# Performance work log

Measured on AMD Instinct MI355X. Metric: run time of the kernel, lower is better.

Reference implementation:

```python
import jax, jax.numpy as jnp
import numpy as np

B, G = 64, 48            # events, grid side -> N = B*G*G nodes
N = B * G * G
DIMS = [128, 102, 73, 44, 16]   # channel schedule from GraphZ defaults
KERN = 3                 # GMM kernels on the conv layer
MAXV = 1.0               # Cartesian(max_value=neighbors=1)


def _build_graph():
    # 3x3 window graph (radius 1, self loops) per event, as in window_edges
    ix, iy = np.meshgrid(np.arange(G), np.arange(G), indexing='ij')
    ix, iy = ix.ravel(), iy.ravel()
    srcs, tgts = [], []
    for dx in (-1, 0, 1):
        for dy in (-1, 0, 1):
            jx, jy = ix + dx, iy + dy
            m = (jx >= 0) & (jx < G) & (jy >= 0) & (jy < G)
            srcs.append(jx[m] * G + jy[m])
            tgts.append(ix[m] * G + iy[m])
    src, tgt = np.concatenate(srcs), np.concatenate(tgts)
    base = (np.arange(B) * G * G)[:, None]
    ei = np.stack([(base + src[None]).ravel(), (base + tgt[None]).ravel()])
    pos = np.stack([np.tile(ix, B).astype(np.float32),
                    np.tile(iy, B).astype(np.float32),
                    np.repeat(np.arange(B), G * G).astype(np.float32)], axis=1)
    return ei.astype(np.int32), pos


def setup_inputs() -> dict:
    key = jax.random.key(0)
    ks = jax.random.split(key, 16)
    ei, pos = _build_graph()
    inp = {
        'x': jax.random.normal(ks[0], (N, DIMS[0]), jnp.float32),
        'pos': jnp.asarray(pos),
        'edge_index': jnp.asarray(ei),
    }
    # pointwise layer 0: 128->102 (+BN)
    inp['w0'] = jax.random.normal(ks[1], (DIMS[0], DIMS[1]), jnp.float32) * (1.0 / np.sqrt(DIMS[0]))
    inp['b0'] = jnp.zeros((DIMS[1],), jnp.float32)
    inp['gamma0'] = jnp.ones((DIMS[1],), jnp.float32)
    inp['beta0'] = jnp.zeros((DIMS[1],), jnp.float32)
    # pointwise layer 1: 102->73 (+BN)
    inp['w1'] = jax.random.normal(ks[2], (DIMS[1], DIMS[2]), jnp.float32) * (1.0 / np.sqrt(DIMS[1]))
    inp['b1'] = jnp.zeros((DIMS[2],), jnp.float32)
    inp['gamma1'] = jnp.ones((DIMS[2],), jnp.float32)
    inp['beta1'] = jnp.zeros((DIMS[2],), jnp.float32)
    # GMM conv layer 2: 73->44, 3 gaussian kernels (+BN)
    inp['w2'] = jax.random.normal(ks[3], (DIMS[2], DIMS[3]), jnp.float32) * (1.0 / np.sqrt(DIMS[2]))
    inp['g2'] = jax.random.normal(ks[4], (DIMS[2], KERN * DIMS[3]), jnp.float32) * (1.0 / np.sqrt(DIMS[2]))
    inp['mu2'] = jax.random.uniform(ks[5], (KERN, 2), jnp.float32)
    inp['sigma2'] = jax.random.uniform(ks[6], (KERN, 2), jnp.float32) + 0.5
    inp['b2'] = jnp.zeros((DIMS[3],), jnp.float32)
    inp['gamma2'] = jnp.ones((DIMS[3],), jnp.float32)
    inp['beta2'] = jnp.zeros((DIMS[3],), jnp.float32)
    # pointwise layer 3: 44->16
    inp['w3'] = jax.random.normal(ks[7], (DIMS[3], DIMS[4]), jnp.float32) * (1.0 / np.sqrt(DIMS[3]))
    inp['b3'] = jnp.zeros((DIMS[4],), jnp.float32)
    return inp


def _bn(x, gamma, beta):
    # BatchNorm1d training forward: biased batch stats over the node dim
    m = jnp.mean(x, axis=0)
    v = jnp.mean((x - m) ** 2, axis=0)
    return (x - m) * jax.lax.rsqrt(v + 1e-5) * gamma + beta


def _gmm_conv(x, ei, ea, g, mu, sigma, w_root, b, n):
    # PyG GMMConv (separate_gaussians=False, aggr='mean', root_weight, bias)
    E = ea.shape[0]
    kk = mu.shape[0]
    out = w_root.shape[1]
    xj = (x @ g)[ei[0]].reshape(E, kk, out)                 # gather transformed src feats
    gauss = jnp.exp(jnp.sum(-0.5 * (ea[:, None, :] - mu[None]) ** 2
                            / (1e-15 + sigma[None] ** 2), axis=-1))  # [E, K]
    msg = jnp.einsum('eko,ek->eo', xj, gauss)               # [E, out]
    s = jax.ops.segment_sum(msg, ei[1], num_segments=n)     # scatter-add to targets
    c = jax.ops.segment_sum(jnp.ones((E,), x.dtype), ei[1], num_segments=n)
    return s / jnp.maximum(c, 1.0)[:, None] + x @ w_root + b


def reference(x, pos, edge_index, w0, b0, gamma0, beta0, w1, b1, gamma1, beta1,
              w2, g2, mu2, sigma2, b2, gamma2, beta2, w3, b3):
    n = x.shape[0]
    pos2 = pos[:, :2]
    # Cartesian(max_value=1, norm=True): pseudo coords in [0, 1]
    ea = (pos2[edge_index[0]] - pos2[edge_index[1]]) / (2.0 * MAXV) + 0.5
    # layers 0,1: knn_graph(k=0) -> empty edge set -> GMMConv = root Linear + bias
    h = _bn(x @ w0 + b0, gamma0, beta0)
    h = _bn(h @ w1 + b1, gamma1, beta1)
    # layer 2: window-edge GMMConv with 3 gaussian kernels
    h = _bn(_gmm_conv(h, edge_index, ea, g2, mu2, sigma2, w2, b2, n), gamma2, beta2)
    # layer 3: pointwise, no norm
    return h @ w3 + b3
```

## Files before the change

kernel.cpp:

```cpp
#include <hip/hip_runtime.h>

#define GRIDW 48
#define NNODES 147456
#define NTILES 2304
#define GB 512

typedef __attribute__((ext_vector_type(8))) short short8;
typedef __attribute__((ext_vector_type(4))) float f32x4;

__device__ inline unsigned short f2bf(float f) {
    union { float f; unsigned u; } v; v.f = f;
    unsigned r = v.u + 0x7FFFu + ((v.u >> 16) & 1u);
    return (unsigned short)(r >> 16);
}
__device__ inline float bf2f(unsigned short h) {
    union { unsigned u; float f; } v; v.u = ((unsigned)h) << 16;
    return v.f;
}

__global__ void prep(const float* __restrict__ w0, const float* __restrict__ b0,
                     const float* __restrict__ w1, const float* __restrict__ b1,
                     const float* __restrict__ g2, const float* __restrict__ w2,
                     const float* __restrict__ b2, const float* __restrict__ w3,
                     const float* __restrict__ b3,
                     unsigned short* __restrict__ wt0, unsigned short* __restrict__ wt1,
                     unsigned short* __restrict__ wt2, unsigned short* __restrict__ wt3,
                     float* __restrict__ biasf0, float* __restrict__ biasf1,
                     float* __restrict__ biasf2, float* __restrict__ biasf3,
                     float* __restrict__ statz) {
    int id = blockIdx.x * 256 + threadIdx.x;
    if (id < 14336) {
        int col = id >> 7, k = id & 127;
        wt0[id] = (col < 102) ? f2bf(w0[k * 102 + col]) : (unsigned short)0;
    } else if (id < 24576) {
        int e = id - 14336; int col = e >> 7, k = e & 127;
        wt1[e] = (col < 73 && k < 102) ? f2bf(w1[k * 73 + col]) : (unsigned short)0;
    } else if (id < 41472) {
        int e = id - 24576; int col = e / 96, k = e - (e / 96) * 96;
        unsigned short v = 0;
        if (k < 73) v = (col < 132) ? f2bf(g2[k * 132 + col]) : f2bf(w2[k * 44 + (col - 132)]);
        wt2[e] = v;
    } else if (id < 42496) {
        int e = id - 41472; int col = e >> 6, k = e & 63;
        wt3[e] = (k < 44) ? f2bf(w3[k * 16 + col]) : (unsigned short)0;
    } else if (id < 42608) { int c = id - 42496; biasf0[c] = (c < 102) ? b0[c] : 0.f; }
    else if (id < 42688) { int c = id - 42608; biasf1[c] = (c < 73) ? b1[c] : 0.f; }
    else if (id < 42864) { int c = id - 42688; biasf2[c] = (c < 132) ? 0.f : b2[c - 132]; }
    else if (id < 42880) { int c = id - 42864; biasf3[c] = b3[c]; }
    else if (id < 43392) { statz[id - 42880] = 0.f; }
}

template<int K, int KP, int MP, int MOUT, int PREVM, int BNSRC,
         bool STATS, bool OUTBF, bool ABF16>
__global__ __launch_bounds__(256) void gemm_p(
    const void* __restrict__ Ain, const unsigned short* __restrict__ WT,
    const float* __restrict__ biasf,
    const float* __restrict__ q0, const float* __restrict__ q1,
    const float* __restrict__ q2, const float* __restrict__ q3,
    float invN, void* __restrict__ Yout,
    float* __restrict__ sumO, float* __restrict__ ssO)
{
    constexpr int KS = KP + 8;
    constexpr int NCF = MP / 16;
    constexpr int UPR = ABF16 ? (K / 8) : (K / 4);
    constexpr int TOT = 64 * UPR;
    constexpr int NLD = (TOT + 255) / 256;
    __shared__ __align__(16) unsigned short As[2][64 * KS];
    __shared__ __align__(16) unsigned short Bs[MP * KS];
    __shared__ float bnA[KP], bnB[KP];

    const int tid = threadIdx.x;
    const int lane = tid & 63, wv = tid >> 6, qd = lane >> 4, lc = lane & 15;

    if (BNSRC == 1) {
        if (tid < KP) {
            float a = 0.f, b = 0.f;
            if (tid < PREVM) {
                float m = q0[tid] * invN;
                float v = q1[tid] * invN - m * m;
                float sc = q2[tid] * rsqrtf(v + 1e-5f);
                a = sc; b = q3[tid] - m * sc;
            }
            bnA[tid] = a; bnB[tid] = b;
        }
    } else if (BNSRC == 2) {
        if (tid < KP) {
            bnA[tid] = (tid < PREVM) ? q0[tid] : 0.f;
            bnB[tid] = (tid < PREVM) ? q1[tid] : 0.f;
        }
    }
    for (int g = tid; g < MP * (KP / 8); g += 256) {
        int col = g / (KP / 8), u = g - col * (KP / 8);
        *(uint4*)&Bs[col * KS + u * 8] = *(const uint4*)&WT[(size_t)col * KP + u * 8];
    }
    if constexpr (KP > K) {
        constexpr int PADU = (KP - K) / 2;
        for (int g = tid; g < 64 * PADU; g += 256) {
            int row = g / PADU, u = g - row * PADU;
            *(unsigned*)&As[0][row * KS + K + u * 2] = 0u;
            *(unsigned*)&As[1][row * KS + K + u * 2] = 0u;
        }
    }

    float bvr[NCF];
#pragma unroll
    for (int cf = 0; cf < NCF; ++cf) bvr[cf] = biasf[cf * 16 + lc];

    float cs[NCF], cq[NCF];
    if (STATS) {
#pragma unroll
        for (int cf = 0; cf < NCF; ++cf) { cs[cf] = 0.f; cq[cf] = 0.f; }
    }

    uint4 pfb[NLD];
    float4 pff[NLD];

    int t = blockIdx.x;
#pragma unroll
    for (int i = 0; i < NLD; ++i) {
        int g = tid + 256 * i;
        if (g < TOT) {
            if constexpr (ABF16)
                pfb[i] = *(const uint4*)((const unsigned short*)Ain + (size_t)t * 64 * K + g * 8);
            else
                pff[i] = *(const float4*)((const float*)Ain + (size_t)t * 64 * K + g * 4);
        }
    }
    __syncthreads();

    int buf = 0;
    for (; t < NTILES; t += GB) {
#pragma unroll
        for (int i = 0; i < NLD; ++i) {
            int g = tid + 256 * i;
            if (g < TOT) {
                int row = g / UPR, u = g - row * UPR;
                if constexpr (ABF16) {
                    uint4 w = pfb[i];
                    if (BNSRC != 0) {
                        unsigned* wp = (unsigned*)&w;
#pragma unroll
                        for (int pp = 0; pp < 4; ++pp) {
                            int kk = u * 8 + 2 * pp;
                            float lo = bf2f((unsigned short)(wp[pp] & 0xFFFFu)) * bnA[kk] + bnB[kk];
                            float hi = bf2f((unsigned short)(wp[pp] >> 16)) * bnA[kk + 1] + bnB[kk + 1];
                            wp[pp] = (unsigned)f2bf(lo) | ((unsigned)f2bf(hi) << 16);
                        }
                    }
                    *(uint4*)&As[buf][row * KS + u * 8] = w;
                } else {
                    float4 v = pff[i];
                    if (BNSRC != 0) {
                        int kk = u * 4;
                        v.x = v.x * bnA[kk] + bnB[kk];
                        v.y = v.y * bnA[kk + 1] + bnB[kk + 1];
                        v.z = v.z * bnA[kk + 2] + bnB[kk + 2];
                        v.w = v.w * bnA[kk + 3] + bnB[kk + 3];
                    }
                    unsigned lo = (unsigned)f2bf(v.x) | ((unsigned)f2bf(v.y) << 16);
                    unsigned hi = (unsigned)f2bf(v.z) | ((unsigned)f2bf(v.w) << 16);
                    *(uint2*)&As[buf][row * KS + u * 4] = make_uint2(lo, hi);
                }
            }
        }
        int t2 = t + GB;
        if (t2 < NTILES) {
#pragma unroll
            for (int i = 0; i < NLD; ++i) {
                int g = tid + 256 * i;
                if (g < TOT) {
                    if constexpr (ABF16)
                        pfb[i] = *(const uint4*)((const unsigned short*)Ain + (size_t)t2 * 64 * K + g * 8);
                    else
                        pff[i] = *(const float4*)((const float*)Ain + (size_t)t2 * 64 * K + g * 4);
                }
            }
        }
        __syncthreads();

        f32x4 acc[NCF];
#pragma unroll
        for (int cf = 0; cf < NCF; ++cf) acc[cf] = (f32x4){0.f, 0.f, 0.f, 0.f};
#pragma unroll
        for (int kt = 0; kt < KP / 32; ++kt) {
            const int kb = kt * 32 + qd * 8;
            short8 a = *(const short8*)&As[buf][(wv * 16 + lc) * KS + kb];
#pragma unroll
            for (int cf = 0; cf < NCF; ++cf) {
                short8 b = *(const short8*)&Bs[(cf * 16 + lc) * KS + kb];
                acc[cf] = __builtin_amdgcn_mfma_f32_16x16x32_bf16(a, b, acc[cf], 0, 0, 0);
            }
        }
#pragma unroll
        for (int cf = 0; cf < NCF; ++cf) {
            const int col = cf * 16 + lc;
            const float bv = bvr[cf];
#pragma unroll
            for (int rr = 0; rr < 4; ++rr) {
                float v = acc[cf][rr] + bv;
                int row = t * 64 + wv * 16 + qd * 4 + rr;
                if (OUTBF) ((unsigned short*)Yout)[(size_t)row * MP + col] = f2bf(v);
                else       ((float*)Yout)[(size_t)row * MP + col] = v;
                if (STATS) { cs[cf] += v; cq[cf] += v * v; }
            }
        }
        buf ^= 1;
    }

    if (STATS) {
        __syncthreads();
        float* red = (float*)As;
        float* redq = red + 4 * MP;
#pragma unroll
        for (int cf = 0; cf < NCF; ++cf) {
            float s = cs[cf], qq = cq[cf];
            s += __shfl_down(s, 32, 64); s += __shfl_down(s, 16, 64);
            qq += __shfl_down(qq, 32, 64); qq += __shfl_down(qq, 16, 64);
            if (lane < 16) {
                red[wv * MP + cf * 16 + lane] = s;
                redq[wv * MP + cf * 16 + lane] = qq;
            }
        }
        __syncthreads();
        if (tid < MOUT) {
            float s = red[tid] + red[MP + tid] + red[2 * MP + tid] + red[3 * MP + tid];
            float qq = redq[tid] + redq[MP + tid] + redq[2 * MP + tid] + redq[3 * MP + tid];
            atomicAdd(&sumO[tid], s);
            atomicAdd(&ssO[tid], qq);
        }
    }
}

__device__ inline void load_u(const unsigned short* __restrict__ TR, int b,
                              int jx, int iy, int c0, const float (*gy)[3],
                              float* __restrict__ u) {
#pragma unroll
    for (int j = 0; j < 12; ++j) u[j] = 0.f;
    if (jx < 0 || jx >= GRIDW) return;
    const unsigned short* rowp = TR + (size_t)(b * 2304 + jx * 48) * 176;
#pragma unroll
    for (int dy = -1; dy <= 1; ++dy) {
        int jy = iy + dy;
        if (jy < 0 || jy >= GRIDW) continue;
        const unsigned short* np = rowp + (size_t)jy * 176 + c0;
#pragma unroll
        for (int k = 0; k < 3; ++k) {
            uint2 v = *(const uint2*)(np + k * 44);
            float g = gy[dy + 1][k];
            u[k * 4 + 0] += g * bf2f((unsigned short)(v.x & 0xFFFFu));
            u[k * 4 + 1] += g * bf2f((unsigned short)(v.x >> 16));
            u[k * 4 + 2] += g * bf2f((unsigned short)(v.y & 0xFFFFu));
            u[k * 4 + 3] += g * bf2f((unsigned short)(v.y >> 16));
        }
    }
}

__global__ __launch_bounds__(256) void gmm_stencil(
    const unsigned short* __restrict__ TR, unsigned short* __restrict__ C,
    const float* __restrict__ mu, const float* __restrict__ sigma,
    float* __restrict__ sum2, float* __restrict__ ss2)
{
    __shared__ float gx[3][3], gy[3][3];
    __shared__ float red[88];
    const int tid = threadIdx.x;
    if (tid < 88) red[tid] = 0.f;
    if (tid < 18) {
        int d = (tid / 3) % 3, k = tid % 3;
        bool isy = tid >= 9;
        float e = 0.5f * (float)(d - 1) + 0.5f;
        float mm = mu[k * 2 + (isy ? 1 : 0)];
        float sg = sigma[k * 2 + (isy ? 1 : 0)];
        float v = expf(-0.5f * (e - mm) * (e - mm) / (1e-15f + sg * sg));
        if (isy) gy[d][k] = v; else gx[d][k] = v;
    }
    __syncthreads();

    const int r = blockIdx.x & 7;
    const int m = blockIdx.x >> 3;
    const int b = r * 8 + (m >> 4);
    const int x0 = (m & 15) * 3;

    for (int p = 0; p < 3; ++p) {
        int idx = tid + 256 * p;
        if (idx >= 528) break;
        int og = idx % 11, iy = idx / 11;
        int c0 = og * 4;
        float u0[12], u1[12], u2[12];
        load_u(TR, b, x0 - 1, iy, c0, gy, u0);
        load_u(TR, b, x0,     iy, c0, gy, u1);
        float s4[4] = {0, 0, 0, 0}, q4[4] = {0, 0, 0, 0};
        int ny = 1 + (iy > 0) + (iy < GRIDW - 1);
#pragma unroll
        for (int st = 0; st < 3; ++st) {
            int ix = x0 + st;
            float* ua = (st == 0) ? u0 : ((st == 1) ? u1 : u2);
            float* ub = (st == 0) ? u1 : ((st == 1) ? u2 : u0);
            float* uc = (st == 0) ? u2 : ((st == 1) ? u0 : u1);
            load_u(TR, b, ix + 1, iy, c0, gy, uc);
            int nx = 1 + (ix > 0) + (ix < GRIDW - 1);
            float inv = 1.f / (float)(nx * ny);
            int node = b * 2304 + ix * 48 + iy;
            uint2 rv = *(const uint2*)(TR + (size_t)node * 176 + 132 + c0);
            float o[4];
#pragma unroll
            for (int j = 0; j < 4; ++j) {
                float acc = 0.f;
#pragma unroll
                for (int k = 0; k < 3; ++k)
                    acc += gx[0][k] * ua[k * 4 + j] + gx[1][k] * ub[k * 4 + j]
                         + gx[2][k] * uc[k * 4 + j];
                o[j] = acc * inv;
            }
            o[0] += bf2f((unsigned short)(rv.x & 0xFFFFu));
            o[1] += bf2f((unsigned short)(rv.x >> 16));
            o[2] += bf2f((unsigned short)(rv.y & 0xFFFFu));
            o[3] += bf2f((unsigned short)(rv.y >> 16));
            unsigned lo = (unsigned)f2bf(o[0]) | ((unsigned)f2bf(o[1]) << 16);
            unsigned hi = (unsigned)f2bf(o[2]) | ((unsigned)f2bf(o[3]) << 16);
            *(uint2*)&C[(size_t)node * 48 + c0] = make_uint2(lo, hi);
            if (og == 10)
                *(uint2*)&C[(size_t)node * 48 + 44] = make_uint2(0u, 0u);
#pragma unroll
            for (int j = 0; j < 4; ++j) { s4[j] += o[j]; q4[j] += o[j] * o[j]; }
        }
#pragma unroll
        for (int j = 0; j < 4; ++j) {
            atomicAdd(&red[c0 + j], s4[j]);
            atomicAdd(&red[44 + c0 + j], q4[j]);
        }
    }
    __syncthreads();
    if (tid < 88)
        atomicAdd(tid < 44 ? &sum2[tid] : &ss2[tid - 44], red[tid]);
}

extern "C" void kernel_launch(void* const* d_in, const int* in_sizes, int n_in,
                              void* d_out, int out_size, void* d_ws, size_t ws_size,
                              hipStream_t stream) {
    const float* x      = (const float*)d_in[0];
    const float* w0     = (const float*)d_in[3];
    const float* b0     = (const float*)d_in[4];
    const float* gamma0 = (const float*)d_in[5];
    const float* beta0  = (const float*)d_in[6];
    const float* w1     = (const float*)d_in[7];
    const float* b1     = (const float*)d_in[8];
    const float* gamma1 = (const float*)d_in[9];
    const float* beta1  = (const float*)d_in[10];
    const float* w2     = (const float*)d_in[11];
    const float* g2     = (const float*)d_in[12];
    const float* mu2    = (const float*)d_in[13];
    const float* sigma2 = (const float*)d_in[14];
    const float* b2     = (const float*)d_in[15];
    const float* gamma2 = (const float*)d_in[16];
    const float* beta2  = (const float*)d_in[17];
    const float* w3     = (const float*)d_in[18];
    const float* b3     = (const float*)d_in[19];
    float* out = (float*)d_out;

    const int N = NNODES;
    const float invN = 1.0f / (float)N;

    const size_t tailOff = (size_t)N * 132;
    size_t need = (tailOff + 300000) * sizeof(float);
    if (ws_size < need) return;

    float* ws = (float*)d_ws;
    unsigned short* bufY1 = (unsigned short*)ws;
    unsigned short* bufC  = (unsigned short*)ws;
    unsigned short* bufY0 = (unsigned short*)(ws + (size_t)N * 44);
    unsigned short* bufTR = bufY0;

    float* tail = ws + tailOff;
    float* sum0 = tail;
    float* ss0  = tail + 112;
    float* sum1 = tail + 224;
    float* ss1  = tail + 304;
    float* sum2 = tail + 384;
    float* ss2  = tail + 448;
    float* biasf0 = tail + 512;
    float* biasf1 = tail + 624;
    float* biasf2 = tail + 704;
    float* biasf3 = tail + 880;
    unsigned short* wt0 = (unsigned short*)(tail + 896);
    unsigned short* wt1 = wt0 + 14336;
    unsigned short* wt2 = wt1 + 10240;
    unsigned short* wt3 = wt2 + 16896;

    prep<<<170, 256, 0, stream>>>(w0, b0, w1, b1, g2, w2, b2, w3, b3,
                                  wt0, wt1, wt2, wt3,
                                  biasf0, biasf1, biasf2, biasf3, tail);

    gemm_p<128, 128, 112, 102, 0, 0, true, true, false><<<GB, 256, 0, stream>>>(
        x, wt0, biasf0, nullptr, nullptr, nullptr, nullptr, invN, bufY0, sum0, ss0);

    gemm_p<112, 128, 80, 73, 102, 1, true, true, true><<<GB, 256, 0, stream>>>(
        bufY0, wt1, biasf1, sum0, ss0, gamma0, beta0, invN, bufY1, sum1, ss1);

    gemm_p<80, 96, 176, 176, 73, 1, false, true, true><<<GB, 256, 0, stream>>>(
        bufY1, wt2, biasf2, sum1, ss1, gamma1, beta1, invN, bufTR, nullptr, nullptr);

    gmm_stencil<<<1024, 256, 0, stream>>>(bufTR, bufC, mu2, sigma2, sum2, ss2);

    gemm_p<48, 64, 16, 16, 44, 1, false, false, true><<<GB, 256, 0, stream>>>(
        bufC, wt3, biasf3, sum2, ss2, gamma2, beta2, invN, out, nullptr, nullptr);
}
```

Before: 276.0 us.

## Shard BN statistic atomics across 8 slots and flatten stencil grid

BatchNorm sum and sum-of-squares accumulators are split into 8 shards indexed by block id, and consumers add the shards back together when computing mean and variance. This spreads global atomic contention across more addresses. The GMM stencil kernel now maps one work item per thread and launches 2112 blocks instead of 1024 blocks each looping three times, which raises parallelism and removes the idle tail iteration. The cost is a larger zeroed stats area and a few extra loads per BN consumer.

```diff
diff --git a/kernel.cpp b/kernel.cpp
--- a/kernel.cpp
+++ b/kernel.cpp
@@ -4,6 +4,8 @@
 #define NNODES 147456
 #define NTILES 2304
 #define GB 512
+#define NSH 8
+#define SHS 128
 
 typedef __attribute__((ext_vector_type(8))) short short8;
 typedef __attribute__((ext_vector_type(4))) float f32x4;
@@ -47,7 +49,7 @@
     else if (id < 42688) { int c = id - 42608; biasf1[c] = (c < 73) ? b1[c] : 0.f; }
     else if (id < 42864) { int c = id - 42688; biasf2[c] = (c < 132) ? 0.f : b2[c - 132]; }
     else if (id < 42880) { int c = id - 42864; biasf3[c] = b3[c]; }
-    else if (id < 43392) { statz[id - 42880] = 0.f; }
+    else if (id < 49024) { statz[id - 42880] = 0.f; }
 }
 
 template<int K, int KP, int MP, int MOUT, int PREVM, int BNSRC,
@@ -76,17 +78,18 @@
         if (tid < KP) {
             float a = 0.f, b = 0.f;
             if (tid < PREVM) {
-                float m = q0[tid] * invN;
-                float v = q1[tid] * invN - m * m;
+                float s0 = 0.f, s1 = 0.f;
+#pragma unroll
+                for (int sh = 0; sh < NSH; ++sh) {
+                    s0 += q0[sh * SHS + tid];
+                    s1 += q1[sh * SHS + tid];
+                }
+                float m = s0 * invN;
+                float v = s1 * invN - m * m;
                 float sc = q2[tid] * rsqrtf(v + 1e-5f);
                 a = sc; b = q3[tid] - m * sc;
             }
             bnA[tid] = a; bnB[tid] = b;
-        }
-    } else if (BNSRC == 2) {
-        if (tid < KP) {
-            bnA[tid] = (tid < PREVM) ? q0[tid] : 0.f;
-            bnB[tid] = (tid < PREVM) ? q1[tid] : 0.f;
         }
     }
     for (int g = tid; g < MP * (KP / 8); g += 256) {
@@ -225,8 +228,9 @@
         if (tid < MOUT) {
             float s = red[tid] + red[MP + tid] + red[2 * MP + tid] + red[3 * MP + tid];
             float qq = redq[tid] + redq[MP + tid] + redq[2 * MP + tid] + redq[3 * MP + tid];
-            atomicAdd(&sumO[tid], s);
-            atomicAdd(&ssO[tid], qq);
+            const int sh = blockIdx.x & (NSH - 1);
+            atomicAdd(&sumO[sh * SHS + tid], s);
+            atomicAdd(&ssO[sh * SHS + tid], qq);
         }
     }
 }
@@ -275,63 +279,65 @@
     }
     __syncthreads();
 
-    const int r = blockIdx.x & 7;
-    const int m = blockIdx.x >> 3;
-    const int b = r * 8 + (m >> 4);
-    const int x0 = (m & 15) * 3;
-
-    for (int p = 0; p < 3; ++p) {
-        int idx = tid + 256 * p;
-        if (idx >= 528) break;
-        int og = idx % 11, iy = idx / 11;
-        int c0 = og * 4;
-        float u0[12], u1[12], u2[12];
-        load_u(TR, b, x0 - 1, iy, c0, gy, u0);
-        load_u(TR, b, x0,     iy, c0, gy, u1);
-        float s4[4] = {0, 0, 0, 0}, q4[4] = {0, 0, 0, 0};
-        int ny = 1 + (iy > 0) + (iy < GRIDW - 1);
-#pragma unroll
-        for (int st = 0; st < 3; ++st) {
-            int ix = x0 + st;
-            float* ua = (st == 0) ? u0 : ((st == 1) ? u1 : u2);
-            float* ub = (st == 0) ? u1 : ((st == 1) ? u2 : u0);
-            float* uc = (st == 0) ? u2 : ((st == 1) ? u0 : u1);
-            load_u(TR, b, ix + 1, iy, c0, gy, uc);
-            int nx = 1 + (ix > 0) + (ix < GRIDW - 1);
-            float inv = 1.f / (float)(nx * ny);
-            int node = b * 2304 + ix * 48 + iy;
-            uint2 rv = *(const uint2*)(TR + (size_t)node * 176 + 132 + c0);
-            float o[4];
-#pragma unroll
-            for (int j = 0; j < 4; ++j) {
-                float acc = 0.f;
-#pragma unroll
-                for (int k = 0; k < 3; ++k)
-                    acc += gx[0][k] * ua[k * 4 + j] + gx[1][k] * ub[k * 4 + j]
-                         + gx[2][k] * uc[k * 4 + j];
-                o[j] = acc * inv;
-            }
-            o[0] += bf2f((unsigned short)(rv.x & 0xFFFFu));
-            o[1] += bf2f((unsigned short)(rv.x >> 16));
-            o[2] += bf2f((unsigned short)(rv.y & 0xFFFFu));
-            o[3] += bf2f((unsigned short)(rv.y >> 16));
-            unsigned lo = (unsigned)f2bf(o[0]) | ((unsigned)f2bf(o[1]) << 16);
-            unsigned hi = (unsigned)f2bf(o[2]) | ((unsigned)f2bf(o[3]) << 16);
-            *(uint2*)&C[(size_t)node * 48 + c0] = make_uint2(lo, hi);
-            if (og == 10)
-                *(uint2*)&C[(size_t)node * 48 + 44] = make_uint2(0u, 0u);
-#pragma unroll
-            for (int j = 0; j < 4; ++j) { s4[j] += o[j]; q4[j] += o[j] * o[j]; }
-        }
+    const int xcd = blockIdx.x & 7;
+    const int bi  = blockIdx.x >> 3;
+    const int b   = xcd * 8 + bi / 33;
+    const unsigned tau = (unsigned)(bi % 33) * 256u + (unsigned)tid;
+    const int og = (int)(tau % 11u);
+    const unsigned r1 = tau / 11u;
+    const int iy = (int)(r1 % 48u);
+    const int x0 = (int)(r1 / 48u) * 3;
+    const int c0 = og * 4;
+
+    float u0[12], u1[12], u2[12];
+    load_u(TR, b, x0 - 1, iy, c0, gy, u0);
+    load_u(TR, b, x0,     iy, c0, gy, u1);
+    float s4[4] = {0, 0, 0, 0}, q4[4] = {0, 0, 0, 0};
+    int ny = 1 + (iy > 0) + (iy < GRIDW - 1);
+#pragma unroll
+    for (int st = 0; st < 3; ++st) {
+        int ix = x0 + st;
+        float* ua = (st == 0) ? u0 : ((st == 1) ? u1 : u2);
+        float* ub = (st == 0) ? u1 : ((st == 1) ? u2 : u0);
+        float* uc = (st == 0) ? u2 : ((st == 1) ? u0 : u1);
+        load_u(TR, b, ix + 1, iy, c0, gy, uc);
+        int nx = 1 + (ix > 0) + (ix < GRIDW - 1);
+        float inv = 1.f / (float)(nx * ny);
+        int node = b * 2304 + ix * 48 + iy;
+        uint2 rv = *(const uint2*)(TR + (size_t)node * 176 + 132 + c0);
+        float o[4];
 #pragma unroll
         for (int j = 0; j < 4; ++j) {
-            atomicAdd(&red[c0 + j], s4[j]);
-            atomicAdd(&red[44 + c0 + j], q4[j]);
-        }
+            float acc = 0.f;
+#pragma unroll
+            for (int k = 0; k < 3; ++k)
+                acc += gx[0][k] * ua[k * 4 + j] + gx[1][k] * ub[k * 4 + j]
+                     + gx[2][k] * uc[k * 4 + j];
+            o[j] = acc * inv;
+        }
+        o[0] += bf2f((unsigned short)(rv.x & 0xFFFFu));
+        o[1] += bf2f((unsigned short)(rv.x >> 16));
+        o[2] += bf2f((unsigned short)(rv.y & 0xFFFFu));
+        o[3] += bf2f((unsigned short)(rv.y >> 16));
+        unsigned lo = (unsigned)f2bf(o[0]) | ((unsigned)f2bf(o[1]) << 16);
+        unsigned hi = (unsigned)f2bf(o[2]) | ((unsigned)f2bf(o[3]) << 16);
+        *(uint2*)&C[(size_t)node * 48 + c0] = make_uint2(lo, hi);
+        if (og == 10)
+            *(uint2*)&C[(size_t)node * 48 + 44] = make_uint2(0u, 0u);
+#pragma unroll
+        for (int j = 0; j < 4; ++j) { s4[j] += o[j]; q4[j] += o[j] * o[j]; }
+    }
+#pragma unroll
+    for (int j = 0; j < 4; ++j) {
+        atomicAdd(&red[c0 + j], s4[j]);
+        atomicAdd(&red[44 + c0 + j], q4[j]);
     }
     __syncthreads();
-    if (tid < 88)
-        atomicAdd(tid < 44 ? &sum2[tid] : &ss2[tid - 44], red[tid]);
+    if (tid < 88) {
+        const int sh = blockIdx.x & (NSH - 1);
+        if (tid < 44) atomicAdd(&sum2[sh * SHS + tid], red[tid]);
+        else          atomicAdd(&ss2[sh * SHS + tid - 44], red[tid]);
+    }
 }
 
 extern "C" void kernel_launch(void* const* d_in, const int* in_sizes, int n_in,
@@ -372,21 +378,21 @@
 
     float* tail = ws + tailOff;
     float* sum0 = tail;
-    float* ss0  = tail + 112;
-    float* sum1 = tail + 224;
-    float* ss1  = tail + 304;
-    float* sum2 = tail + 384;
-    float* ss2  = tail + 448;
-    float* biasf0 = tail + 512;
-    float* biasf1 = tail + 624;
-    float* biasf2 = tail + 704;
-    float* biasf3 = tail + 880;
-    unsigned short* wt0 = (unsigned short*)(tail + 896);
+    float* ss0  = tail + 1024;
+    float* sum1 = tail + 2048;
+    float* ss1  = tail + 3072;
+    float* sum2 = tail + 4096;
+    float* ss2  = tail + 5120;
+    float* biasf0 = tail + 6144;
+    float* biasf1 = tail + 6256;
+    float* biasf2 = tail + 6336;
+    float* biasf3 = tail + 6512;
+    unsigned short* wt0 = (unsigned short*)(tail + 6528);
     unsigned short* wt1 = wt0 + 14336;
     unsigned short* wt2 = wt1 + 10240;
     unsigned short* wt3 = wt2 + 16896;
 
-    prep<<<170, 256, 0, stream>>>(w0, b0, w1, b1, g2, w2, b2, w3, b3,
+    prep<<<192, 256, 0, stream>>>(w0, b0, w1, b1, g2, w2, b2, w3, b3,
                                   wt0, wt1, wt2, wt3,
                                   biasf0, biasf1, biasf2, biasf3, tail);
 
@@ -399,7 +405,7 @@
     gemm_p<80, 96, 176, 176, 73, 1, false, true, true><<<GB, 256, 0, stream>>>(
         bufY1, wt2, biasf2, sum1, ss1, gamma1, beta1, invN, bufTR, nullptr, nullptr);
 
-    gmm_stencil<<<1024, 256, 0, stream>>>(bufTR, bufC, mu2, sigma2, sum2, ss2);
+    gmm_stencil<<<2112, 256, 0, stream>>>(bufTR, bufC, mu2, sigma2, sum2, ss2);
 
     gemm_p<48, 64, 16, 16, 44, 1, false, false, true><<<GB, 256, 0, stream>>>(
         bufC, wt3, biasf3, sum2, ss2, gamma2, beta2, invN, out, nullptr, nullptr);
```

Result: faster. 248.7 us (-9.9%).
